# Kernel tuning notes

Hardware: AMD Instinct MI355X
Metric: run time of the kernel (lower is better)

## Reference

```python
import jax, jax.numpy as jnp
import numpy as np

D_MODEL, NUM_HEADS, ROPE_DIM = 256, 8, 16
B_GRAPHS, N_MAX = 16, 512


def _make_batch():
    # ragged graph sizes between 256 and 512 atoms; contiguous, sorted ids
    sizes = np.array([256 + (i * 256) // 15 for i in range(B_GRAPHS)], dtype=np.int64)
    return np.repeat(np.arange(B_GRAPHS), sizes)  # total N = 6137


def setup_inputs() -> dict:
    key = jax.random.key(0)
    ks = jax.random.split(key, 6)
    batch_np = _make_batch()
    N = int(batch_np.shape[0])
    x = jax.random.normal(ks[0], (N, D_MODEL), jnp.float32)
    pos = jax.random.normal(ks[1], (N, 3), jnp.float32) * 3.0
    W_qkv = jax.random.normal(ks[2], (D_MODEL, 3 * D_MODEL), jnp.float32) / np.sqrt(D_MODEL).astype(np.float32)
    W_out = jax.random.normal(ks[3], (D_MODEL, D_MODEL), jnp.float32) / np.sqrt(D_MODEL).astype(np.float32)
    rope_freqs = jax.random.normal(ks[4], (ROPE_DIM,), jnp.float32) * 0.1
    W_rope = jax.random.normal(ks[5], (ROPE_DIM, NUM_HEADS), jnp.float32) / np.sqrt(ROPE_DIM).astype(np.float32)
    gamma = jnp.ones((D_MODEL,), jnp.float32)
    beta = jnp.zeros((D_MODEL,), jnp.float32)
    return {"x": x, "pos": pos, "batch": jnp.asarray(batch_np, jnp.int32),
            "W_qkv": W_qkv, "W_out": W_out, "rope_freqs": rope_freqs,
            "W_rope": W_rope, "gamma": gamma, "beta": beta,
            "B": B_GRAPHS, "n_max": N_MAX}


def _forward(x, pos, W_qkv, W_out, rope_freqs, W_rope, gamma, beta, batch, B, n_max):
    N, d = x.shape
    H = W_rope.shape[1]
    hd = d // H
    scale = hd ** -0.5
    # pad ragged graphs to [B, n_max] via vectorized scatter (batch is sorted)
    sizes = jax.ops.segment_sum(jnp.ones((N,), jnp.int32), batch, num_segments=B)
    offsets = jnp.concatenate([jnp.zeros((1,), jnp.int32), jnp.cumsum(sizes)[:-1].astype(jnp.int32)])
    pidx = jnp.arange(N, dtype=jnp.int32) - offsets[batch]  # position within graph
    x_pad = jnp.zeros((B, n_max, d), x.dtype).at[batch, pidx].set(x)
    pos_pad = jnp.zeros((B, n_max, 3), pos.dtype).at[batch, pidx].set(pos)
    pad = jnp.ones((B, n_max), bool).at[batch, pidx].set(False)  # True = padding
    # multi-head self-attention on scalar channel
    qkv = x_pad @ W_qkv  # [B, n, 3d]
    q, k, v = jnp.split(qkv, 3, axis=-1)
    heads = lambda t: t.reshape(B, n_max, H, hd).transpose(0, 2, 1, 3)  # [B,H,n,hd]
    q, k, v = heads(q), heads(k), heads(v)
    logits = jnp.einsum('bhid,bhjd->bhij', q, k) * scale
    # Euclidean RoPE distance bias: rope_proj(cos(|omega| * ||r_i - r_j||))
    diff = pos_pad[:, :, None, :] - pos_pad[:, None, :, :]  # [B,n,n,3]
    sq = jnp.sum(diff * diff, axis=-1)
    dist = jnp.where(sq > 0, jnp.sqrt(jnp.where(sq > 0, sq, 1.0)), 0.0)  # safe norm
    fourier = jnp.cos(dist[..., None] * jnp.abs(rope_freqs))  # [B,n,n,r]
    bias = jnp.einsum('bijr,rh->bhij', fourier, W_rope)
    pair_pad = (pad[:, :, None] | pad[:, None, :])[:, None]  # [B,1,n,n]
    bias = jnp.where(pair_pad, 0.0, bias)
    logits = jnp.where(pad[:, None, None, :], -1e9, logits + bias)
    attn = jax.nn.softmax(logits, axis=-1)
    out = jnp.einsum('bhij,bhjd->bhid', attn, v)
    out = out.transpose(0, 2, 1, 3).reshape(B, n_max, d) @ W_out
    out_flat = out[batch, pidx]  # gather back to flat node list
    # residual + LayerNorm (eps = 1e-5)
    y = x + out_flat
    mu = jnp.mean(y, axis=-1, keepdims=True)
    var = jnp.mean((y - mu) ** 2, axis=-1, keepdims=True)
    return gamma * (y - mu) * jax.lax.rsqrt(var + 1e-5) + beta


def reference(x, pos, batch, W_qkv, W_out, rope_freqs, W_rope, gamma, beta, B, n_max):
    return _forward(x, pos, W_qkv, W_out, rope_freqs, W_rope, gamma, beta, batch, B, n_max)
```

## Files before the change

kernel.cpp:

```cpp
#include <hip/hip_runtime.h>
#include <hip/hip_bf16.h>

typedef __hip_bfloat16 bf16;
typedef short bf16x8 __attribute__((ext_vector_type(8)));
typedef float f32x4 __attribute__((ext_vector_type(4)));

#define NGRAPH 16
#define QSCALE 0.17677669529663687f
#define VT_LD 8192

__device__ __forceinline__ bf16x8 ldcvt8(const float* p) {
  float4 u = *(const float4*)p, v = *(const float4*)(p + 4);
  __align__(16) bf16 tmp[8];
  tmp[0] = __float2bfloat16(u.x); tmp[1] = __float2bfloat16(u.y);
  tmp[2] = __float2bfloat16(u.z); tmp[3] = __float2bfloat16(u.w);
  tmp[4] = __float2bfloat16(v.x); tmp[5] = __float2bfloat16(v.y);
  tmp[6] = __float2bfloat16(v.z); tmp[7] = __float2bfloat16(v.w);
  return *(const bf16x8*)tmp;
}

__global__ __launch_bounds__(256) void k_pre(const float* __restrict__ Wqkv,
                                             const float* __restrict__ Wout,
                                             const int* __restrict__ batch,
                                             const float* __restrict__ freqs,
                                             const float* __restrict__ Wrope,
                                             bf16* __restrict__ Wqkv_t,
                                             bf16* __restrict__ Wout_t,
                                             float* __restrict__ Tblg,
                                             int* __restrict__ offs, int N) {
  __shared__ float ld[64][65];
  int bid = blockIdx.x, t = threadIdx.x;
  int c = t & 63, r0 = t >> 6;
  if (bid < 48) {
    int k0 = (bid & 3) * 64, n0 = (bid >> 2) * 64;
    #pragma unroll
    for (int r = r0; r < 64; r += 4) ld[r][c] = Wqkv[(size_t)(k0 + r) * 768 + n0 + c];
    __syncthreads();
    #pragma unroll
    for (int r = r0; r < 64; r += 4)
      Wqkv_t[(size_t)(n0 + r) * 256 + k0 + c] = __float2bfloat16(ld[c][r]);
  } else if (bid < 64) {
    int b2 = bid - 48;
    int k0 = (b2 & 3) * 64, n0 = (b2 >> 2) * 64;
    #pragma unroll
    for (int r = r0; r < 64; r += 4) ld[r][c] = Wout[(size_t)(k0 + r) * 256 + n0 + c];
    __syncthreads();
    #pragma unroll
    for (int r = r0; r < 64; r += 4)
      Wout_t[(size_t)(n0 + r) * 256 + k0 + c] = __float2bfloat16(ld[c][r]);
  } else if (bid == 64) {
    for (int i = t; i < N; i += 256) {
      if (i == 0) { offs[0] = 0; offs[NGRAPH] = N; }
      else if (batch[i] != batch[i - 1]) offs[batch[i]] = i;
    }
  } else {
    int i = (bid - 65) * 256 + t;
    if (i < 384) {
      float d = i * 0.125f;
      float a[8];
      #pragma unroll
      for (int h = 0; h < 8; ++h) a[h] = 0.f;
      #pragma unroll
      for (int r = 0; r < 16; ++r) {
        float cv = __cosf(d * fabsf(freqs[r]));
        #pragma unroll
        for (int h = 0; h < 8; ++h) a[h] += cv * Wrope[r * 8 + h];
      }
      #pragma unroll
      for (int h = 0; h < 8; ++h) Tblg[i * 8 + h] = a[h];
    }
  }
}

__global__ __launch_bounds__(256) void k_gemm(const float* __restrict__ x,
                                              const bf16* __restrict__ Wqkv_t,
                                              const int* __restrict__ batch,
                                              const int* __restrict__ offs,
                                              bf16* __restrict__ QKVb,
                                              bf16* __restrict__ VT, int N) {
  __shared__ float tr[64][33];
  __shared__ int rowcol[32];
  int t = threadIdx.x;
  int w = t >> 6, l = t & 63, fr = l & 15, fq = l >> 4;
  int rh = w & 1, ch = w >> 1;
  int m0 = blockIdx.x * 32, n0 = blockIdx.y * 64;
  if (t < 32) {
    int m = m0 + t; if (m > N - 1) m = N - 1;
    int b = batch[m];
    rowcol[t] = b * 512 + (m - offs[b]);
  }
  int arow = m0 + rh * 16 + fr; if (arow > N - 1) arow = N - 1;
  bf16x8 af[8];
  #pragma unroll
  for (int kt = 0; kt < 8; ++kt)
    af[kt] = ldcvt8(x + (size_t)arow * 256 + kt * 32 + fq * 8);
  #pragma unroll
  for (int p = 0; p < 3; ++p) {
    f32x4 acc[2];
    #pragma unroll
    for (int nt = 0; nt < 2; ++nt) {
      acc[nt] = (f32x4){0.f, 0.f, 0.f, 0.f};
      int brow = p * 256 + n0 + ch * 32 + nt * 16 + fr;
      #pragma unroll
      for (int kt = 0; kt < 8; ++kt) {
        bf16x8 bf_ = *(const bf16x8*)(Wqkv_t + (size_t)brow * 256 + kt * 32 + fq * 8);
        acc[nt] = __builtin_amdgcn_mfma_f32_16x16x32_bf16(af[kt], bf_, acc[nt], 0, 0, 0);
      }
    }
    float sc = (p == 0) ? QSCALE : 1.f;
    #pragma unroll
    for (int nt = 0; nt < 2; ++nt) {
      int col = p * 256 + n0 + ch * 32 + nt * 16 + fr;
      #pragma unroll
      for (int rr = 0; rr < 4; ++rr) {
        int m = m0 + rh * 16 + fq * 4 + rr;
        if (m < N) QKVb[(size_t)m * 768 + col] = __float2bfloat16(acc[nt][rr] * sc);
      }
    }
    if (p == 2) {
      #pragma unroll
      for (int nt = 0; nt < 2; ++nt)
        #pragma unroll
        for (int rr = 0; rr < 4; ++rr)
          tr[ch * 32 + nt * 16 + fr][rh * 16 + fq * 4 + rr] = acc[nt][rr];
      __syncthreads();
      int c = t >> 2, rr0 = (t & 3) * 8;
      int dg = n0 + c;
      #pragma unroll
      for (int i = 0; i < 8; ++i) {
        int r = rr0 + i;
        VT[(size_t)dg * VT_LD + rowcol[r]] = __float2bfloat16(tr[c][r]);
      }
    }
  }
}

__global__ __launch_bounds__(256) void k_attn(const float* __restrict__ pos,
                                              const float* __restrict__ Tblg,
                                              const bf16* __restrict__ QKVb,
                                              const bf16* __restrict__ VT,
                                              const int* __restrict__ offs,
                                              float* __restrict__ Op,
                                              float* __restrict__ lp, int N, int JC) {
  __shared__ unsigned int T2u[1536];
  __shared__ float px[512], py[512], pz[512];
  __shared__ __align__(16) bf16 Pt[4][16][40];
  int b = blockIdx.y, jc = blockIdx.z;
  int off = offs[b], n = offs[b + 1] - off;
  int q0 = blockIdx.x * 16;
  if (q0 >= n) return;
  int t = threadIdx.x, w = t >> 6, l = t & 63, fr = l & 15, fq = l >> 4;

  for (int e = t; e < 1536; e += 256) {
    int i = e >> 2, hp = e & 3;
    bf16 blo = __float2bfloat16(Tblg[i * 8 + hp]);
    bf16 bhi = __float2bfloat16(Tblg[i * 8 + hp + 4]);
    unsigned short ulo = *(unsigned short*)&blo, uhi = *(unsigned short*)&bhi;
    T2u[e] = (unsigned)ulo | ((unsigned)uhi << 16);
  }
  int n3 = n * 3;
  for (int idx = t; idx < n3; idx += 256) {
    float v = pos[(size_t)off * 3 + idx];
    int slot = idx / 3, c = idx - slot * 3;
    if (c == 0) px[slot] = v; else if (c == 1) py[slot] = v; else pz[slot] = v;
  }

  int h0 = w, h1 = w + 4;
  const bf16* Kb0 = QKVb + (size_t)off * 768 + 256 + h0 * 32 + fq * 8;
  const bf16* Kb1 = QKVb + (size_t)off * 768 + 256 + h1 * 32 + fq * 8;
  const bf16* Vb0 = VT + (size_t)(h0 * 32 + fr) * VT_LD + b * 512 + fq * 8;
  const bf16* Vb1 = VT + (size_t)(h1 * 32 + fr) * VT_LD + b * 512 + fq * 8;
  int qrow = q0 + fr; bool qv = qrow < n;
  size_t qoff = (size_t)(qv ? off + qrow : off) * 768 + fq * 8;
  bf16x8 aq[2];
  aq[0] = *(const bf16x8*)(QKVb + qoff + h0 * 32);
  aq[1] = *(const bf16x8*)(QKVb + qoff + h1 * 32);
  if (!qv) { aq[0] = (bf16x8){0,0,0,0,0,0,0,0}; aq[1] = aq[0]; }

  __syncthreads();

  float qx[4], qy[4], qz[4];
  #pragma unroll
  for (int rr = 0; rr < 4; ++rr) {
    int qq = q0 + fq * 4 + rr; if (qq >= n) qq = n - 1;
    qx[rr] = px[qq]; qy[rr] = py[qq]; qz[rr] = pz[qq];
  }

  f32x4 Oa[2][2];
  Oa[0][0] = (f32x4){0.f,0.f,0.f,0.f}; Oa[0][1] = Oa[0][0];
  Oa[1][0] = Oa[0][0];                 Oa[1][1] = Oa[0][0];
  float lacc[2][4] = {{0.f,0.f,0.f,0.f},{0.f,0.f,0.f,0.f}};
  int jtiles = (n + 31) >> 5;
  int jt0 = (jtiles * jc) / JC, jt1 = (jtiles * (jc + 1)) / JC;

  for (int jt = jt0; jt < jt1; ++jt) {
    int k0 = jt * 32 + fr, k1 = k0 + 16;
    size_t r0 = (size_t)((k0 < n) ? k0 : 0) * 768;
    size_t r1 = (size_t)((k1 < n) ? k1 : 0) * 768;
    bf16x8 ck00 = *(const bf16x8*)(Kb0 + r0), ck01 = *(const bf16x8*)(Kb0 + r1);
    bf16x8 ck10 = *(const bf16x8*)(Kb1 + r0), ck11 = *(const bf16x8*)(Kb1 + r1);
    bf16x8 cv00 = *(const bf16x8*)(Vb0 + jt * 32);
    bf16x8 cv01 = *(const bf16x8*)(Vb0 + (size_t)16 * VT_LD + jt * 32);
    bf16x8 cv10 = *(const bf16x8*)(Vb1 + jt * 32);
    bf16x8 cv11 = *(const bf16x8*)(Vb1 + (size_t)16 * VT_LD + jt * 32);

    bool vj0 = k0 < n, vj1 = k1 < n;
    int js0 = vj0 ? k0 : 0, js1 = vj1 ? k1 : 0;
    float jx0 = px[js0], jy0 = py[js0], jz0 = pz[js0];
    float jx1 = px[js1], jy1 = py[js1], jz1 = pz[js1];
    float bias[2][2][4];
    #pragma unroll
    for (int rr = 0; rr < 4; ++rr) {
      {
        float dx = qx[rr] - jx0, dy = qy[rr] - jy0, dz = qz[rr] - jz0;
        float fi = sqrtf(dx * dx + dy * dy + dz * dz) * 8.0f;
        int i = (int)fi; if (i > 382) i = 382;
        float f2 = fi - (float)i;
        unsigned ua = T2u[i * 4 + w], ub = T2u[i * 4 + 4 + w];
        float la = __uint_as_float(ua << 16), ha = __uint_as_float(ua & 0xffff0000u);
        float lb = __uint_as_float(ub << 16), hb = __uint_as_float(ub & 0xffff0000u);
        bias[0][0][rr] = vj0 ? (la + f2 * (lb - la)) : -1e30f;
        bias[0][1][rr] = vj0 ? (ha + f2 * (hb - ha)) : -1e30f;
      }
      {
        float dx = qx[rr] - jx1, dy = qy[rr] - jy1, dz = qz[rr] - jz1;
        float fi = sqrtf(dx * dx + dy * dy + dz * dz) * 8.0f;
        int i = (int)fi; if (i > 382) i = 382;
        float f2 = fi - (float)i;
        unsigned ua = T2u[i * 4 + w], ub = T2u[i * 4 + 4 + w];
        float la = __uint_as_float(ua << 16), ha = __uint_as_float(ua & 0xffff0000u);
        float lb = __uint_as_float(ub << 16), hb = __uint_as_float(ub & 0xffff0000u);
        bias[1][0][rr] = vj1 ? (la + f2 * (lb - la)) : -1e30f;
        bias[1][1][rr] = vj1 ? (ha + f2 * (hb - ha)) : -1e30f;
      }
    }

    #pragma unroll
    for (int hh = 0; hh < 2; ++hh) {
      f32x4 z = {0.f, 0.f, 0.f, 0.f};
      f32x4 S0 = __builtin_amdgcn_mfma_f32_16x16x32_bf16(aq[hh], hh ? ck10 : ck00, z, 0, 0, 0);
      f32x4 S1 = __builtin_amdgcn_mfma_f32_16x16x32_bf16(aq[hh], hh ? ck11 : ck01, z, 0, 0, 0);
      #pragma unroll
      for (int k = 0; k < 8; ++k) {
        int jti = k >> 2, rr = k & 3;
        float s = (jti ? S1[rr] : S0[rr]) + bias[jti][hh][rr];
        float p = __expf(s);
        lacc[hh][rr] += p;
        Pt[w][fq * 4 + rr][jti * 16 + fr] = __float2bfloat16(p);
      }
      bf16x8 ap = *(const bf16x8*)&Pt[w][fr][fq * 8];
      Oa[hh][0] = __builtin_amdgcn_mfma_f32_16x16x32_bf16(ap, hh ? cv10 : cv00, Oa[hh][0], 0, 0, 0);
      Oa[hh][1] = __builtin_amdgcn_mfma_f32_16x16x32_bf16(ap, hh ? cv11 : cv01, Oa[hh][1], 0, 0, 0);
    }
  }

  #pragma unroll
  for (int hh = 0; hh < 2; ++hh)
    #pragma unroll
    for (int rr = 0; rr < 4; ++rr) {
      #pragma unroll
      for (int m2 = 1; m2 <= 8; m2 <<= 1) lacc[hh][rr] += __shfl_xor(lacc[hh][rr], m2);
    }
  float* Opc = Op + (size_t)jc * N * 256;
  float* lpc = lp + (size_t)jc * N * 8;
  #pragma unroll
  for (int hh = 0; hh < 2; ++hh) {
    int h = w + 4 * hh;
    #pragma unroll
    for (int rr = 0; rr < 4; ++rr) {
      int row = q0 + fq * 4 + rr;
      if (row < n) {
        #pragma unroll
        for (int dh = 0; dh < 2; ++dh)
          Opc[(size_t)(off + row) * 256 + h * 32 + dh * 16 + fr] = Oa[hh][dh][rr];
        if (fr == 0) lpc[(size_t)(off + row) * 8 + h] = lacc[hh][rr];
      }
    }
  }
}

__global__ __launch_bounds__(256) void k_out_ln(const float* __restrict__ Op,
                                                const float* __restrict__ lp,
                                                const bf16* __restrict__ Bt,
                                                const float* __restrict__ x,
                                                const float* __restrict__ gamma,
                                                const float* __restrict__ beta,
                                                float* __restrict__ out, int M, int JC) {
  __shared__ float ps[4][16], pss[4][16];
  int t = threadIdx.x, w = t >> 6, l = t & 63, fr = l & 15, fq = l >> 4;
  int m0 = blockIdx.x * 16;
  int arow = m0 + fr; if (arow > M - 1) arow = M - 1;
  float linv[8];
  {
    float ls[8] = {0.f,0.f,0.f,0.f,0.f,0.f,0.f,0.f};
    for (int c = 0; c < JC; ++c) {
      const float* p = lp + ((size_t)c * M + arow) * 8;
      float4 a0 = *(const float4*)p, a1 = *(const float4*)(p + 4);
      ls[0] += a0.x; ls[1] += a0.y; ls[2] += a0.z; ls[3] += a0.w;
      ls[4] += a1.x; ls[5] += a1.y; ls[6] += a1.z; ls[7] += a1.w;
    }
    #pragma unroll
    for (int h = 0; h < 8; ++h) linv[h] = 1.f / ls[h];
  }
  bf16x8 af[8];
  #pragma unroll
  for (int kt = 0; kt < 8; ++kt) {
    size_t o = (size_t)arow * 256 + kt * 32 + fq * 8;
    float s0 = 0.f, s1 = 0.f, s2 = 0.f, s3 = 0.f, s4 = 0.f, s5 = 0.f, s6 = 0.f, s7 = 0.f;
    for (int c = 0; c < JC; ++c) {
      const float* p = Op + (size_t)c * M * 256 + o;
      float4 u = *(const float4*)p, v = *(const float4*)(p + 4);
      s0 += u.x; s1 += u.y; s2 += u.z; s3 += u.w;
      s4 += v.x; s5 += v.y; s6 += v.z; s7 += v.w;
    }
    float li = linv[kt];
    __align__(16) bf16 tmp[8];
    tmp[0] = __float2bfloat16(s0 * li); tmp[1] = __float2bfloat16(s1 * li);
    tmp[2] = __float2bfloat16(s2 * li); tmp[3] = __float2bfloat16(s3 * li);
    tmp[4] = __float2bfloat16(s4 * li); tmp[5] = __float2bfloat16(s5 * li);
    tmp[6] = __float2bfloat16(s6 * li); tmp[7] = __float2bfloat16(s7 * li);
    af[kt] = *(const bf16x8*)tmp;
  }
  f32x4 acc[4];
  #pragma unroll
  for (int nt = 0; nt < 4; ++nt) {
    acc[nt] = (f32x4){0.f, 0.f, 0.f, 0.f};
    int brow = w * 64 + nt * 16 + fr;
    #pragma unroll
    for (int kt = 0; kt < 8; ++kt) {
      bf16x8 bf_ = *(const bf16x8*)(Bt + (size_t)brow * 256 + kt * 32 + fq * 8);
      acc[nt] = __builtin_amdgcn_mfma_f32_16x16x32_bf16(af[kt], bf_, acc[nt], 0, 0, 0);
    }
  }
  float y[4][4];
  #pragma unroll
  for (int rr = 0; rr < 4; ++rr) {
    int row = m0 + fq * 4 + rr;
    int rc = (row < M) ? row : (M - 1);
    float s = 0.f, ss = 0.f;
    #pragma unroll
    for (int nt = 0; nt < 4; ++nt) {
      float v = acc[nt][rr] + x[(size_t)rc * 256 + w * 64 + nt * 16 + fr];
      y[rr][nt] = v; s += v; ss += v * v;
    }
    #pragma unroll
    for (int m2 = 1; m2 <= 8; m2 <<= 1) { s += __shfl_xor(s, m2); ss += __shfl_xor(ss, m2); }
    if (fr == 0) { ps[w][fq * 4 + rr] = s; pss[w][fq * 4 + rr] = ss; }
  }
  __syncthreads();
  #pragma unroll
  for (int rr = 0; rr < 4; ++rr) {
    int row = m0 + fq * 4 + rr;
    int ri = fq * 4 + rr;
    float s = ps[0][ri] + ps[1][ri] + ps[2][ri] + ps[3][ri];
    float ss = pss[0][ri] + pss[1][ri] + pss[2][ri] + pss[3][ri];
    float mean = s * (1.f / 256.f);
    float var = ss * (1.f / 256.f) - mean * mean;
    float rstd = rsqrtf(var + 1e-5f);
    if (row < M) {
      #pragma unroll
      for (int nt = 0; nt < 4; ++nt) {
        int col = w * 64 + nt * 16 + fr;
        out[(size_t)row * 256 + col] = gamma[col] * (y[rr][nt] - mean) * rstd + beta[col];
      }
    }
  }
}

extern "C" void kernel_launch(void* const* d_in, const int* in_sizes, int n_in,
                              void* d_out, int out_size, void* d_ws, size_t ws_size,
                              hipStream_t stream) {
  (void)n_in; (void)out_size;
  const float* x     = (const float*)d_in[0];
  const float* pos   = (const float*)d_in[1];
  const int*   batch = (const int*)d_in[2];
  const float* Wqkv  = (const float*)d_in[3];
  const float* Wout  = (const float*)d_in[4];
  const float* freqs = (const float*)d_in[5];
  const float* Wrope = (const float*)d_in[6];
  const float* gamma = (const float*)d_in[7];
  const float* beta  = (const float*)d_in[8];
  float* out = (float*)d_out;

  int N = in_sizes[0] / 256;

  int JC = (ws_size >= (size_t)41 * 1024 * 1024) ? 4 : 2;

  char* base = (char*)d_ws;
  int*   offs   = (int*)base;
  bf16*  QKVb   = (bf16*)(base + 1024);
  bf16*  VT     = (bf16*)(base + 9427456);
  bf16*  Wqkv_t = (bf16*)(base + 13621760);
  bf16*  Wout_t = (bf16*)(base + 14014976);
  float* Tblg   = (float*)(base + 14146048);
  float* Op     = (float*)(base + 14158336);
  float* lp     = (float*)(base + 14158336 + (size_t)JC * N * 1024);

  int MBm = (N + 31) / 32;
  k_pre<<<67, 256, 0, stream>>>(Wqkv, Wout, batch, freqs, Wrope, Wqkv_t, Wout_t, Tblg, offs, N);
  k_gemm<<<dim3(MBm, 4), 256, 0, stream>>>(x, Wqkv_t, batch, offs, QKVb, VT, N);
  k_attn<<<dim3(32, NGRAPH, JC), 256, 0, stream>>>(pos, Tblg, QKVb, VT, offs, Op, lp, N, JC);
  k_out_ln<<<(N + 15) / 16, 256, 0, stream>>>(Op, lp, Wout_t, x, gamma, beta, out, N, JC);
}
```

Before: 180.3 us.

## Precompute pairwise RoPE bias tiles in separate kernel before attention

Adds a k_bias kernel that computes the distance-based interpolated bias (and padding mask) for every 16x32 query/key tile. It writes the result to a global bf16 buffer laid out to match the MFMA fragment order. A new attention kernel reads these tiles instead of loading positions and doing sqrt and table interpolation inline. The goal is to strip scalar bias work out of the attention inner loop, at the cost of tens of MB of extra global write and read traffic. This path is only taken when the workspace is at least 70MB, and it then fixes the key-chunk split JC at 2.

```diff
diff --git a/kernel.cpp b/kernel.cpp
--- a/kernel.cpp
+++ b/kernel.cpp
@@ -8,6 +8,8 @@
 #define NGRAPH 16
 #define QSCALE 0.17677669529663687f
 #define VT_LD 8192
+
+struct __align__(16) bf8x { bf16 v[8]; };
 
 __device__ __forceinline__ bf16x8 ldcvt8(const float* p) {
   float4 u = *(const float4*)p, v = *(const float4*)(p + 4);
@@ -18,6 +20,8 @@
   tmp[6] = __float2bfloat16(v.z); tmp[7] = __float2bfloat16(v.w);
   return *(const bf16x8*)tmp;
 }
+
+__device__ __forceinline__ float b2f(bf16 v) { return __bfloat162float(v); }
 
 __global__ __launch_bounds__(256) void k_pre(const float* __restrict__ Wqkv,
                                              const float* __restrict__ Wout,
@@ -135,13 +139,172 @@
   }
 }
 
-__global__ __launch_bounds__(256) void k_attn(const float* __restrict__ pos,
+__global__ __launch_bounds__(256) void k_bias(const float* __restrict__ pos,
                                               const float* __restrict__ Tblg,
-                                              const bf16* __restrict__ QKVb,
-                                              const bf16* __restrict__ VT,
                                               const int* __restrict__ offs,
-                                              float* __restrict__ Op,
-                                              float* __restrict__ lp, int N, int JC) {
+                                              bf16* __restrict__ Sbg) {
+  int qt = blockIdx.x, b = blockIdx.y, jt = blockIdx.z;
+  int off = offs[b], n = offs[b + 1] - off;
+  if (qt * 16 >= n || jt * 32 >= n) return;
+  int tbase = 0;
+  for (int g = 0; g < b; ++g) {
+    int ng = offs[g + 1] - offs[g];
+    tbase += ((ng + 15) >> 4) * ((ng + 31) >> 5);
+  }
+  int jtiles = (n + 31) >> 5;
+  size_t tile = (size_t)(tbase + qt * jtiles + jt) * 4096;
+
+  __shared__ unsigned T2u[1536];
+  __shared__ __align__(16) bf16 Sbf[8][64][8];
+  int t = threadIdx.x;
+  for (int e = t; e < 1536; e += 256) {
+    int i = e >> 2, hp = e & 3;
+    bf16 bl = __float2bfloat16(Tblg[i * 8 + hp]);
+    bf16 bh = __float2bfloat16(Tblg[i * 8 + hp + 4]);
+    T2u[e] = (unsigned)*(unsigned short*)&bl | ((unsigned)*(unsigned short*)&bh << 16);
+  }
+  __syncthreads();
+
+  int bq = t >> 5, bj = t & 31;
+  int jg = jt * 32 + bj; bool vj = jg < n;
+  int a = (vj ? off + jg : off) * 3;
+  float jx = pos[a], jy = pos[a + 1], jz = pos[a + 2];
+  #pragma unroll
+  for (int e = 0; e < 2; ++e) {
+    int q = bq + 8 * e;
+    int qq = qt * 16 + q; bool bqv = qq < n;
+    int L = (q >> 2) * 16 + (bj & 15);
+    int k = (bj >> 4) * 4 + (q & 3);
+    if (vj && bqv) {
+      int aq_ = (off + qq) * 3;
+      float dx = pos[aq_] - jx, dy = pos[aq_ + 1] - jy, dz = pos[aq_ + 2] - jz;
+      float fi = sqrtf(dx * dx + dy * dy + dz * dz) * 8.0f;
+      int i = (int)fi; if (i > 382) i = 382;
+      float f2 = fi - (float)i;
+      #pragma unroll
+      for (int hp = 0; hp < 4; ++hp) {
+        unsigned ua = T2u[i * 4 + hp], ub = T2u[i * 4 + 4 + hp];
+        float la = __uint_as_float(ua << 16), ha = __uint_as_float(ua & 0xffff0000u);
+        float lb = __uint_as_float(ub << 16), hb = __uint_as_float(ub & 0xffff0000u);
+        Sbf[hp][L][k]     = __float2bfloat16(la + f2 * (lb - la));
+        Sbf[hp + 4][L][k] = __float2bfloat16(ha + f2 * (hb - ha));
+      }
+    } else {
+      bf16 s = __float2bfloat16(vj ? 0.f : -1e30f);
+      #pragma unroll
+      for (int h = 0; h < 8; ++h) Sbf[h][L][k] = s;
+    }
+  }
+  __syncthreads();
+  const bf16x8* src = (const bf16x8*)&Sbf[0][0][0];
+  bf16x8* dst = (bf16x8*)(Sbg + tile);
+  dst[t] = src[t]; dst[t + 256] = src[t + 256];
+}
+
+__global__ __launch_bounds__(256) void k_attn_pb(const bf16* __restrict__ QKVb,
+                                                 const bf16* __restrict__ VT,
+                                                 const bf16* __restrict__ Sbg,
+                                                 const int* __restrict__ offs,
+                                                 float* __restrict__ Op,
+                                                 float* __restrict__ lp, int N, int JC) {
+  __shared__ __align__(16) bf16 Pt[4][16][40];
+  int b = blockIdx.y, jc = blockIdx.z;
+  int off = offs[b], n = offs[b + 1] - off;
+  int q0 = blockIdx.x * 16;
+  if (q0 >= n) return;
+  int t = threadIdx.x, w = t >> 6, l = t & 63, fr = l & 15, fq = l >> 4;
+
+  int tbase = 0;
+  for (int g = 0; g < b; ++g) {
+    int ng = offs[g + 1] - offs[g];
+    tbase += ((ng + 15) >> 4) * ((ng + 31) >> 5);
+  }
+  int jtiles = (n + 31) >> 5;
+  const bf16* Sb0 = Sbg + (size_t)(tbase + (q0 >> 4) * jtiles) * 4096 + w * 512 + l * 8;
+
+  int h0 = w, h1 = w + 4;
+  const bf16* Kb0 = QKVb + (size_t)off * 768 + 256 + h0 * 32 + fq * 8;
+  const bf16* Kb1 = QKVb + (size_t)off * 768 + 256 + h1 * 32 + fq * 8;
+  const bf16* Vb0 = VT + (size_t)(h0 * 32 + fr) * VT_LD + b * 512 + fq * 8;
+  const bf16* Vb1 = VT + (size_t)(h1 * 32 + fr) * VT_LD + b * 512 + fq * 8;
+  int qrow = q0 + fr; bool qv = qrow < n;
+  size_t qoff = (size_t)(qv ? off + qrow : off) * 768 + fq * 8;
+  bf16x8 aq[2];
+  aq[0] = *(const bf16x8*)(QKVb + qoff + h0 * 32);
+  aq[1] = *(const bf16x8*)(QKVb + qoff + h1 * 32);
+  if (!qv) { aq[0] = (bf16x8){0,0,0,0,0,0,0,0}; aq[1] = aq[0]; }
+
+  f32x4 Oa[2][2];
+  Oa[0][0] = (f32x4){0.f,0.f,0.f,0.f}; Oa[0][1] = Oa[0][0];
+  Oa[1][0] = Oa[0][0];                 Oa[1][1] = Oa[0][0];
+  float lacc[2][4] = {{0.f,0.f,0.f,0.f},{0.f,0.f,0.f,0.f}};
+  int jt0 = (jtiles * jc) / JC, jt1 = (jtiles * (jc + 1)) / JC;
+
+  for (int jt = jt0; jt < jt1; ++jt) {
+    int k0 = jt * 32 + fr, k1 = k0 + 16;
+    size_t r0 = (size_t)((k0 < n) ? k0 : 0) * 768;
+    size_t r1 = (size_t)((k1 < n) ? k1 : 0) * 768;
+    bf16x8 ck00 = *(const bf16x8*)(Kb0 + r0), ck01 = *(const bf16x8*)(Kb0 + r1);
+    bf16x8 ck10 = *(const bf16x8*)(Kb1 + r0), ck11 = *(const bf16x8*)(Kb1 + r1);
+    bf16x8 cv00 = *(const bf16x8*)(Vb0 + jt * 32);
+    bf16x8 cv01 = *(const bf16x8*)(Vb0 + (size_t)16 * VT_LD + jt * 32);
+    bf16x8 cv10 = *(const bf16x8*)(Vb1 + jt * 32);
+    bf16x8 cv11 = *(const bf16x8*)(Vb1 + (size_t)16 * VT_LD + jt * 32);
+    bf8x bb0 = *(const bf8x*)(Sb0 + (size_t)jt * 4096);
+    bf8x bb1 = *(const bf8x*)(Sb0 + (size_t)jt * 4096 + 4 * 512);
+
+    #pragma unroll
+    for (int hh = 0; hh < 2; ++hh) {
+      f32x4 z = {0.f, 0.f, 0.f, 0.f};
+      f32x4 S0 = __builtin_amdgcn_mfma_f32_16x16x32_bf16(aq[hh], hh ? ck10 : ck00, z, 0, 0, 0);
+      f32x4 S1 = __builtin_amdgcn_mfma_f32_16x16x32_bf16(aq[hh], hh ? ck11 : ck01, z, 0, 0, 0);
+      bf8x bb = hh ? bb1 : bb0;
+      #pragma unroll
+      for (int k = 0; k < 8; ++k) {
+        int jti = k >> 2, rr = k & 3;
+        float s = (jti ? S1[rr] : S0[rr]) + b2f(bb.v[k]);
+        float p = __expf(s);
+        lacc[hh][rr] += p;
+        Pt[w][fq * 4 + rr][jti * 16 + fr] = __float2bfloat16(p);
+      }
+      bf16x8 ap = *(const bf16x8*)&Pt[w][fr][fq * 8];
+      Oa[hh][0] = __builtin_amdgcn_mfma_f32_16x16x32_bf16(ap, hh ? cv10 : cv00, Oa[hh][0], 0, 0, 0);
+      Oa[hh][1] = __builtin_amdgcn_mfma_f32_16x16x32_bf16(ap, hh ? cv11 : cv01, Oa[hh][1], 0, 0, 0);
+    }
+  }
+
+  #pragma unroll
+  for (int hh = 0; hh < 2; ++hh)
+    #pragma unroll
+    for (int rr = 0; rr < 4; ++rr) {
+      #pragma unroll
+      for (int m2 = 1; m2 <= 8; m2 <<= 1) lacc[hh][rr] += __shfl_xor(lacc[hh][rr], m2);
+    }
+  float* Opc = Op + (size_t)jc * N * 256;
+  float* lpc = lp + (size_t)jc * N * 8;
+  #pragma unroll
+  for (int hh = 0; hh < 2; ++hh) {
+    int h = w + 4 * hh;
+    #pragma unroll
+    for (int rr = 0; rr < 4; ++rr) {
+      int row = q0 + fq * 4 + rr;
+      if (row < n) {
+        #pragma unroll
+        for (int dh = 0; dh < 2; ++dh)
+          Opc[(size_t)(off + row) * 256 + h * 32 + dh * 16 + fr] = Oa[hh][dh][rr];
+        if (fr == 0) lpc[(size_t)(off + row) * 8 + h] = lacc[hh][rr];
+      }
+    }
+  }
+}
+
+__global__ __launch_bounds__(256) void k_attn_il(const float* __restrict__ pos,
+                                                 const float* __restrict__ Tblg,
+                                                 const bf16* __restrict__ QKVb,
+                                                 const bf16* __restrict__ VT,
+                                                 const int* __restrict__ offs,
+                                                 float* __restrict__ Op,
+                                                 float* __restrict__ lp, int N, int JC) {
   __shared__ unsigned int T2u[1536];
   __shared__ float px[512], py[512], pz[512];
   __shared__ __align__(16) bf16 Pt[4][16][40];
@@ -155,8 +318,7 @@
     int i = e >> 2, hp = e & 3;
     bf16 blo = __float2bfloat16(Tblg[i * 8 + hp]);
     bf16 bhi = __float2bfloat16(Tblg[i * 8 + hp + 4]);
-    unsigned short ulo = *(unsigned short*)&blo, uhi = *(unsigned short*)&bhi;
-    T2u[e] = (unsigned)ulo | ((unsigned)uhi << 16);
+    T2u[e] = (unsigned)*(unsigned short*)&blo | ((unsigned)*(unsigned short*)&bhi << 16);
   }
   int n3 = n * 3;
   for (int idx = t; idx < n3; idx += 256) {
@@ -384,7 +546,8 @@
 
   int N = in_sizes[0] / 256;
 
-  int JC = (ws_size >= (size_t)41 * 1024 * 1024) ? 4 : 2;
+  bool PB = ws_size >= (size_t)70 * 1024 * 1024;
+  int JC = PB ? 2 : ((ws_size >= (size_t)41 * 1024 * 1024) ? 4 : 2);
 
   char* base = (char*)d_ws;
   int*   offs   = (int*)base;
@@ -395,10 +558,16 @@
   float* Tblg   = (float*)(base + 14146048);
   float* Op     = (float*)(base + 14158336);
   float* lp     = (float*)(base + 14158336 + (size_t)JC * N * 1024);
+  bf16*  Sbg    = (bf16*)(base + 27120640);
 
   int MBm = (N + 31) / 32;
   k_pre<<<67, 256, 0, stream>>>(Wqkv, Wout, batch, freqs, Wrope, Wqkv_t, Wout_t, Tblg, offs, N);
   k_gemm<<<dim3(MBm, 4), 256, 0, stream>>>(x, Wqkv_t, batch, offs, QKVb, VT, N);
-  k_attn<<<dim3(32, NGRAPH, JC), 256, 0, stream>>>(pos, Tblg, QKVb, VT, offs, Op, lp, N, JC);
+  if (PB) {
+    k_bias<<<dim3(32, NGRAPH, 16), 256, 0, stream>>>(pos, Tblg, offs, Sbg);
+    k_attn_pb<<<dim3(32, NGRAPH, JC), 256, 0, stream>>>(QKVb, VT, Sbg, offs, Op, lp, N, JC);
+  } else {
+    k_attn_il<<<dim3(32, NGRAPH, JC), 256, 0, stream>>>(pos, Tblg, QKVb, VT, offs, Op, lp, N, JC);
+  }
   k_out_ln<<<(N + 15) / 16, 256, 0, stream>>>(Op, lp, Wout_t, x, gamma, beta, out, N, JC);
 }
```

After: 184.6 us. +2.4%, slower.
